# Kernel tuning notes

Measured on AMD Instinct MI355X. Metric: run time of the kernel, lower is better.

The kernel has to match this reference:

```python
import jax, jax.numpy as jnp
import numpy as np
from jax import lax

B, N, D = 32, 256, 128  # graphs, nodes-per-graph, embed_dim
T = B * N               # total nodes


def _mlp(x, W1, b1, W2, b2):
    # Linear -> ReLU -> Linear (query_proj / key_proj)
    return jnp.maximum(x @ W1.T + b1, 0.0) @ W2.T + b2


def _l2norm(x):
    # F.normalize(dim=-1), eps=1e-12
    return x / jnp.maximum(jnp.linalg.norm(x, axis=-1, keepdims=True), 1e-12)


def _gru_cell(x, h, W_ih, W_hh, b_ih, b_hh):
    # torch.nn.GRU single-step cell, gate order (r, z, n)
    gi = x @ W_ih.T + b_ih
    gh = h @ W_hh.T + b_hh
    ir, iz, inn = jnp.split(gi, 3, axis=-1)
    hr, hz, hn = jnp.split(gh, 3, axis=-1)
    r = jax.nn.sigmoid(ir + hr)
    z = jax.nn.sigmoid(iz + hz)
    n = jnp.tanh(inn + r * hn)
    return (1.0 - z) * n + z * h


def setup_inputs() -> dict:
    key = jax.random.key(0)
    ks = jax.random.split(key, 16)
    s = float(1.0 / np.sqrt(D))
    u = lambda k, sh: jax.random.uniform(k, sh, jnp.float32, -s, s)
    return {
        "node_embeddings": jax.random.normal(ks[0], (T, D), jnp.float32),
        "start_nodes": jnp.arange(B, dtype=jnp.int32) * N,  # first node of each graph
        "batch_idx": jnp.repeat(jnp.arange(B, dtype=jnp.int32), N),
        "Wq1": u(ks[1], (D, D)), "bq1": u(ks[2], (D,)),
        "Wq2": u(ks[3], (D, D)), "bq2": u(ks[4], (D,)),
        "Wk1": u(ks[5], (D, D)), "bk1": u(ks[6], (D,)),
        "Wk2": u(ks[7], (D, D)), "bk2": u(ks[8], (D,)),
        "W_ih": u(ks[9], (3 * D, D)), "W_hh": u(ks[10], (3 * D, D)),
        "b_ih": u(ks[11], (3 * D,)), "b_hh": u(ks[12], (3 * D,)),
        "v": jax.random.normal(ks[13], (D,), jnp.float32),
        "Wh": u(ks[14], (D, D)), "bh": u(ks[15], (D,)),
    }


def reference(node_embeddings, start_nodes, batch_idx, Wq1, bq1, Wq2, bq2,
              Wk1, bk1, Wk2, bk2, W_ih, W_hh, b_ih, b_hh, v, Wh, bh):
    Bn = start_nodes.shape[0]
    Tn = node_embeddings.shape[0]
    steps = Tn // Bn - 1  # equal-size graphs: N-1 decode steps after start node

    # graph contexts = per-graph mean of node embeddings -> hidden init
    ones = jnp.ones((Tn,), jnp.float32)
    counts = jax.ops.segment_sum(ones, batch_idx, num_segments=Bn)
    gctx = jax.ops.segment_sum(node_embeddings, batch_idx, num_segments=Bn) / counts[:, None]
    hidden0 = gctx @ Wh.T + bh                       # [B, D]

    # keys are recomputed identically every step in torch; hoist (same math)
    keys = _l2norm(_mlp(node_embeddings, Wk1, bk1, Wk2, bk2))  # [T, D]
    member = batch_idx[None, :] == jnp.arange(Bn)[:, None]     # [B, T]

    def step(carry, _):
        hidden, current, mask = carry
        mask = mask.at[current].set(False)           # visit current nodes
        x = node_embeddings[current]                 # [B, D]
        h = _gru_cell(x, hidden, W_ih, W_hh, b_ih, b_hh)
        q = _l2norm(_mlp(h, Wq1, bq1, Wq2, bq2))     # [B, D]
        # scores over ALL nodes, then masked to own-graph unvisited (as in torch)
        scores = jnp.einsum('btd,d->bt', jnp.tanh(keys[None] + q[:, None, :]), v)
        valid = member & mask[None, :]
        scores = jnp.where(valid, scores, -jnp.inf)
        probs = jax.nn.softmax(scores, axis=1)
        logp = jnp.log(probs + 1e-10)
        nxt = jnp.argmax(probs, axis=1).astype(current.dtype)  # eval-mode greedy
        lp = jnp.take_along_axis(logp, nxt[:, None], axis=1)[:, 0]
        return (h, nxt, mask), (current, lp)

    init = (hidden0, start_nodes, jnp.ones((Tn,), bool))
    (_, cur, _), (tour_steps, lps) = lax.scan(jax.checkpoint(step), init, None, length=steps)
    tours = jnp.concatenate([tour_steps, cur[None]], axis=0).T  # [B, N]
    log_probs = lps.T                                           # [B, N-1]
    return tours, log_probs
```

## Files before the change

### kernel.cpp

```cpp
#include <hip/hip_runtime.h>
#include <hip/hip_bf16.h>
#include <math.h>

#define DD   128
#define NPG  256
#define NGR  32
#define TTOT 8192
#define LOG2E  1.4426950408889634f
#define LOG2E2 2.8853900817779268f
#define KSTRIDE 264
#define SSTR    268
#define H2A(j)  ((j) + (((j)>>5)<<3))
#define PAD16(j) ((j) + (((j)>>4)<<2))

__device__ __forceinline__ float dot4(float4 a, float4 b){
  return a.x*b.x + a.y*b.y + a.z*b.z + a.w*b.w;
}
template<int CTRL, int RMASK>
__device__ __forceinline__ float upd_f(float oldv, float x){
  return __int_as_float(__builtin_amdgcn_update_dpp(
      __float_as_int(oldv), __float_as_int(x), CTRL, RMASK, 0xf, false));
}
__device__ __forceinline__ float dpp_xor1(float x){
  return __int_as_float(__builtin_amdgcn_mov_dpp(__float_as_int(x), 0xB1, 0xf, 0xf, false));
}
__device__ __forceinline__ float dpp_xor2(float x){
  return __int_as_float(__builtin_amdgcn_mov_dpp(__float_as_int(x), 0x4E, 0xf, 0xf, false));
}
__device__ __forceinline__ float quad_sum_dpp(float x){
  float s = x + dpp_xor1(x);
  return s + dpp_xor2(s);
}
__device__ __forceinline__ float dpp_wave_sum(float x){
  x += upd_f<0x111,0xf>(0.f, x);
  x += upd_f<0x112,0xf>(0.f, x);
  x += upd_f<0x114,0xf>(0.f, x);
  x += upd_f<0x118,0xf>(0.f, x);
  x += upd_f<0x142,0xa>(0.f, x);
  x += upd_f<0x143,0xc>(0.f, x);
  return __uint_as_float(__builtin_amdgcn_readlane(__float_as_uint(x), 63));
}
__device__ __forceinline__ float dpp_wave_max(float x){
  const float NI = -INFINITY;
  x = fmaxf(x, upd_f<0x111,0xf>(NI, x));
  x = fmaxf(x, upd_f<0x112,0xf>(NI, x));
  x = fmaxf(x, upd_f<0x114,0xf>(NI, x));
  x = fmaxf(x, upd_f<0x118,0xf>(NI, x));
  x = fmaxf(x, upd_f<0x142,0xa>(NI, x));
  x = fmaxf(x, upd_f<0x143,0xc>(NI, x));
  return __uint_as_float(__builtin_amdgcn_readlane(__float_as_uint(x), 63));
}
__device__ __forceinline__ float sigfast(float x){
  return __builtin_amdgcn_rcpf(1.f + __builtin_amdgcn_exp2f(-x*LOG2E));
}
__device__ __forceinline__ float tanhfast(float y){
  return 1.f - 2.f*__builtin_amdgcn_rcpf(1.f + __builtin_amdgcn_exp2f(y*LOG2E2));
}


__device__ __forceinline__ void load_w128(float* Ws, const float* __restrict__ W, int t){
  const float4* src = (const float4*)W;
  #pragma unroll
  for (int m=0;m<16;m++){
    int idx = m*256+t; int r = idx>>5, c4 = idx&31;
    float4 val = src[idx];
    float* dst = &Ws[r*129 + c4*4];
    dst[0]=val.x; dst[1]=val.y; dst[2]=val.z; dst[3]=val.w;
  }
}

__device__ __forceinline__ void mm_tile(const float* __restrict__ inS, const float* __restrict__ Ws,
                                        float acc[4][4], int jg, int ng){
  #pragma unroll
  for(int r=0;r<4;r++)
    #pragma unroll
    for(int c=0;c<4;c++) acc[r][c]=0.f;
  #pragma unroll 4
  for (int k=0;k<128;k++){
    float w[4], x[4];
    #pragma unroll
    for (int r=0;r<4;r++) w[r] = Ws[(jg*4+r)*129+k];
    #pragma unroll
    for (int c=0;c<4;c++) x[c] = inS[(ng*4+c)*129+k];
    #pragma unroll
    for (int r=0;r<4;r++)
      #pragma unroll
      for (int c=0;c<4;c++) acc[r][c] += w[r]*x[c];
  }
}

__global__ __launch_bounds__(256) void precompute_kernel(
    const float* __restrict__ emb,
    const float* __restrict__ Wk1, const float* __restrict__ bk1,
    const float* __restrict__ Wk2, const float* __restrict__ bk2,
    const float* __restrict__ Wih, const float* __restrict__ bih,
    float* __restrict__ keysE, float* __restrict__ giall)
{
  __shared__ __align__(16) float xs[32*129];
  __shared__ __align__(16) float Ws[128*129];
  __shared__ __align__(16) float hs[32*129];
  __shared__ __align__(16) float os[32*129];
  __shared__ float nrm[32];
  const int t  = threadIdx.x;
  const int n0 = blockIdx.x * 32;
  const int ng = t & 7, jg = t >> 3;

  {
    const float4* src = (const float4*)emb + (size_t)n0*32;
    #pragma unroll
    for (int m=0;m<4;m++){
      int idx = m*256+t; int n = idx>>5, c4 = idx&31;
      float4 val = src[idx];
      float* dst = &xs[n*129 + c4*4];
      dst[0]=val.x; dst[1]=val.y; dst[2]=val.z; dst[3]=val.w;
    }
  }
  load_w128(Ws, Wk1, t);
  __syncthreads();
  {
    float acc[4][4];
    mm_tile(xs, Ws, acc, jg, ng);
    #pragma unroll
    for (int r=0;r<4;r++){
      float bb = bk1[jg*4+r];
      #pragma unroll
      for (int c=0;c<4;c++) hs[(ng*4+c)*129 + jg*4+r] = fmaxf(acc[r][c]+bb, 0.f);
    }
  }
  __syncthreads();
  load_w128(Ws, Wk2, t);
  __syncthreads();
  {
    float acc[4][4];
    mm_tile(hs, Ws, acc, jg, ng);
    #pragma unroll
    for (int r=0;r<4;r++){
      float bb = bk2[jg*4+r];
      #pragma unroll
      for (int c=0;c<4;c++) os[(ng*4+c)*129 + jg*4+r] = acc[r][c]+bb;
    }
  }
  __syncthreads();
  if (t<32){
    float ss=0.f;
    for (int j=0;j<128;j++){ float x = os[t*129+j]; ss += x*x; }
    nrm[t] = fmaxf(sqrtf(ss), 1e-12f);
  }
  __syncthreads();
  #pragma unroll
  for (int m=0;m<16;m++){
    int idx = m*256+t; int nl = idx & 31, d = idx >> 5;
    float kk = os[nl*129 + d] / nrm[nl];
    keysE[(size_t)d*TTOT + n0 + nl] = __builtin_amdgcn_exp2f(kk * LOG2E2);
  }
  for (int c=0;c<3;c++){
    __syncthreads();
    load_w128(Ws, Wih + c*16384, t);
    __syncthreads();
    float acc[4][4];
    mm_tile(xs, Ws, acc, jg, ng);
    #pragma unroll
    for (int r=0;r<4;r++){
      float bb = bih[c*128 + jg*4+r];
      #pragma unroll
      for (int cc=0;cc<4;cc++)
        giall[(size_t)(n0 + ng*4+cc)*384 + c*128 + jg*4 + r] = acc[r][cc] + bb;
    }
  }
}


__global__ __launch_bounds__(512, 2) void decode_kernel(
    const float* __restrict__ emb,
    const float* __restrict__ keysE, const float* __restrict__ giall,
    const float* __restrict__ Whh, const float* __restrict__ bhh,
    const float* __restrict__ Wq1, const float* __restrict__ bq1,
    const float* __restrict__ Wq2, const float* __restrict__ bq2,
    const float* __restrict__ v,   const float* __restrict__ Wh,
    const float* __restrict__ bh,  const int* __restrict__ start_nodes,
    float* __restrict__ tours_o, float* __restrict__ lp_o)
{
  __shared__ __align__(16) float keys_s[128*KSTRIDE];
  __shared__ __align__(16) float h_s[2][160];
  __shared__ __align__(16) float qh_s[160];
  __shared__ __align__(16) float q_s[160];
  __shared__ __align__(16) float v_sp[160];
  __shared__ __align__(16) float spartS[8*SSTR];
  __shared__ int col2node_s[256], node2col_s[256];
  __shared__ float red2[8];

  const int t = threadIdx.x;
  const int b = blockIdx.x;
  const int g  = t >> 2, s3 = t & 3;
  const int w  = t >> 6, L  = t & 63;
  const int oct = L & 7, dgrp = L >> 3;

  float4 whh4[3][8], wq14[8], wq24[8];
  {
    const float4* w0  = (const float4*)(Whh + (size_t)(g      )*128 + s3*32);
    const float4* w1  = (const float4*)(Whh + (size_t)(128 + g)*128 + s3*32);
    const float4* w2  = (const float4*)(Whh + (size_t)(256 + g)*128 + s3*32);
    const float4* q1p = (const float4*)(Wq1 + (size_t)g*128 + s3*32);
    const float4* q2p = (const float4*)(Wq2 + (size_t)g*128 + s3*32);
    #pragma unroll
    for (int i=0;i<8;i++){
      whh4[0][i]=w0[i]; whh4[1][i]=w1[i]; whh4[2][i]=w2[i];
      wq14[i]=q1p[i];   wq24[i]=q2p[i];
    }
  }
  const float br = bhh[g], bz = bhh[128+g], bn = bhh[256+g];
  const float b1g = bq1[g], b2g = bq2[g];

  if (t<128) v_sp[PAD16(t)] = -2.f * v[t];
  if (t<256){ col2node_s[t] = t; node2col_s[t] = t; }
  {
    #pragma unroll
    for (int m=0;m<16;m++){
      int idx = m*512 + t; int d = idx>>6, q = idx&63;
      *(float4*)(keys_s + d*KSTRIDE + q*4) =
        *(const float4*)(keysE + (size_t)d*TTOT + b*256 + q*4);
    }
  }
  {
    int d = t & 127, part = t >> 7;
    float a = 0.f;
    const float* base = emb + (size_t)(b*256 + part*64)*128 + d;
    for (int i=0;i<64;i++) a += base[(size_t)i*128];
    spartS[part*128+d] = a;
  }
  int cur = start_nodes[b];
  __syncthreads();
  if (t<128){
    float a = 0.f;
    #pragma unroll
    for (int p=0;p<4;p++) a += spartS[p*128+t];
    q_s[t] = a * (1.f/256.f);
  }
  __syncthreads();
  if (t<128){
    float a = bh[t];
    const float* wr = Wh + (size_t)t*128;
    for (int k=0;k<128;k++) a += wr[k]*q_s[k];
    h_s[0][H2A(t)] = a;
  }
  {
    float xv = (t<128) ? v[t] : 0.f;
    float tot = dpp_wave_sum(xv);
    if (L==0) red2[w] = tot;
  }
  __syncthreads();
  float sv = 0.f;
  #pragma unroll
  for (int i=0;i<8;i++) sv += red2[i];

  float gir=0.f, giz=0.f, gin=0.f;
  if (s3==0){
    const float* gp = giall + (size_t)cur*384 + g;
    gir = gp[0]; giz = gp[128]; gin = gp[256];
  }

  for (int step=0; step<255; step++){
    const int par = step & 1;
    const int V   = 255 - step;
    const int curl = cur - b*256;

    if (t >= 128 && t < 256){
      int r = t - 128;
      int px = node2col_s[curl];
      keys_s[r*KSTRIDE + px] = keys_s[r*KSTRIDE + V];
    }
    if (t == 384) tours_o[b*256+step] = (float)cur;

    {
      float a0=0.f,a1=0.f,a2=0.f;
      const float4* hc4 = (const float4*)(h_s[par] + s3*40);
      #pragma unroll
      for (int i=0;i<8;i++){
        float4 hv = hc4[i];
        a0 += dot4(whh4[0][i], hv);
        a1 += dot4(whh4[1][i], hv);
        a2 += dot4(whh4[2][i], hv);
      }
      a0 = quad_sum_dpp(a0);
      a1 = quad_sum_dpp(a1);
      a2 = quad_sum_dpp(a2);
      if (s3==0){
        float r = sigfast(gir + a0 + br);
        float z = sigfast(giz + a1 + bz);
        float n = tanhfast(gin + r*(a2 + bn));
        h_s[par^1][H2A(g)] = (1.f-z)*n + z*h_s[par][H2A(g)];
      }
    }
    __syncthreads();

    if (t == 448){
      int px = node2col_s[curl];
      int ln = col2node_s[V];
      col2node_s[px] = ln;
      node2col_s[ln] = px;
    }

    {
      float a=0.f;
      const float4* hc4 = (const float4*)(h_s[par^1] + s3*40);
      #pragma unroll
      for (int i=0;i<8;i++) a += dot4(wq14[i], hc4[i]);
      a = quad_sum_dpp(a);
      if (s3==0) qh_s[H2A(g)] = fmaxf(a + b1g, 0.f);
    }
    __syncthreads();

    {
      float a=0.f;
      const float4* qc4 = (const float4*)(qh_s + s3*40);
      #pragma unroll
      for (int i=0;i<8;i++) a += dot4(wq24[i], qc4[i]);
      a = quad_sum_dpp(a);
      float qval = a + b2g;
      if (s3==0) q_s[PAD16(g)] = qval;
      float ssp = (s3==0) ? qval*qval : 0.f;
      float tot = dpp_wave_sum(ssp);
      if (L==0) red2[w] = tot;
    }
    __syncthreads();

    if (32*w < V){
      float ss = 0.f;
      #pragma unroll
      for (int i=0;i<8;i++) ss += red2[i];
      float rn = 1.f / fmaxf(sqrtf(ss), 1e-12f);
      const float* kbase = keys_s + dgrp*16*KSTRIDE + 32*w + oct*4;
      const float* qb    = q_s  + dgrp*20;
      const float* vbase = v_sp + dgrp*20;
      float4 acc = {0.f,0.f,0.f,0.f};
      #pragma unroll
      for (int jj=0;jj<16;jj++){
        float eqj = __builtin_amdgcn_exp2f(qb[jj] * rn * LOG2E2);
        float vj  = vbase[jj];
        float4 K = *(const float4*)(kbase + jj*KSTRIDE);
        float r0 = __builtin_amdgcn_rcpf(fmaf(K.x, eqj, 1.f));
        float r1 = __builtin_amdgcn_rcpf(fmaf(K.y, eqj, 1.f));
        float r2 = __builtin_amdgcn_rcpf(fmaf(K.z, eqj, 1.f));
        float r3 = __builtin_amdgcn_rcpf(fmaf(K.w, eqj, 1.f));
        acc.x = fmaf(vj, r0, acc.x);
        acc.y = fmaf(vj, r1, acc.y);
        acc.z = fmaf(vj, r2, acc.z);
        acc.w = fmaf(vj, r3, acc.w);
      }
      *(float4*)(spartS + dgrp*SSTR + 32*w + oct*4) = acc;
    }
    __syncthreads();

    {
      const float* sp = spartS + 4*L;
      float sx=0.f, sy=0.f, sz=0.f, sw=0.f;
      #pragma unroll
      for (int i=0;i<8;i++){
        float4 p = *(const float4*)(sp + i*SSTR);
        sx += p.x; sy += p.y; sz += p.z; sw += p.w;
      }
      int c0 = 4*L;
      float vx = (c0+0 < V) ? sv+sx : -INFINITY;
      float vy = (c0+1 < V) ? sv+sy : -INFINITY;
      float vz = (c0+2 < V) ? sv+sz : -INFINITY;
      float vw = (c0+3 < V) ? sv+sw : -INFINITY;
      float bm = vx; int bc = c0;
      if (vy > bm){ bm=vy; bc=c0+1; }
      if (vz > bm){ bm=vz; bc=c0+2; }
      if (vw > bm){ bm=vw; bc=c0+3; }
      float m = dpp_wave_max(bm);
      unsigned long long mk = __ballot(bm == m);
      int flane = __ffsll(mk) - 1;
      int besti = __builtin_amdgcn_readlane(bc, flane);
      float es = __builtin_amdgcn_exp2f((vx-m)*LOG2E) + __builtin_amdgcn_exp2f((vy-m)*LOG2E)
               + __builtin_amdgcn_exp2f((vz-m)*LOG2E) + __builtin_amdgcn_exp2f((vw-m)*LOG2E);
      float S = dpp_wave_sum(es);
      cur = b*256 + col2node_s[besti];
      if (s3==0){
        const float* gp = giall + (size_t)cur*384 + g;
        gir = gp[0]; giz = gp[128]; gin = gp[256];
      }
      if (t==320) lp_o[b*255+step] = logf(1.f/S + 1e-10f);
    }
  }
  if (t==0) tours_o[b*256+255] = (float)cur;

  (void)oct;
}

extern "C" void kernel_launch(void* const* d_in, const int* in_sizes, int n_in,
                              void* d_out, int out_size, void* d_ws, size_t ws_size,
                              hipStream_t stream) {
  const float* emb  = (const float*)d_in[0];
  const int*   startn = (const int*)d_in[1];
  const float* Wq1 = (const float*)d_in[3];  const float* bq1 = (const float*)d_in[4];
  const float* Wq2 = (const float*)d_in[5];  const float* bq2 = (const float*)d_in[6];
  const float* Wk1 = (const float*)d_in[7];  const float* bk1 = (const float*)d_in[8];
  const float* Wk2 = (const float*)d_in[9];  const float* bk2 = (const float*)d_in[10];
  const float* Wih = (const float*)d_in[11]; const float* Whh = (const float*)d_in[12];
  const float* bih = (const float*)d_in[13]; const float* bhh = (const float*)d_in[14];
  const float* v   = (const float*)d_in[15]; const float* Wh  = (const float*)d_in[16];
  const float* bh  = (const float*)d_in[17];

  float* keysE = (float*)d_ws;
  float* giall = keysE + (size_t)TTOT*DD;

  float* outp = (float*)d_out;

  precompute_kernel<<<256, 256, 0, stream>>>(emb, Wk1, bk1, Wk2, bk2, Wih, bih, keysE, giall);
  decode_kernel<<<NGR, 512, 0, stream>>>(emb, keysE, giall, Whh, bhh, Wq1, bq1, Wq2, bq2,
                                         v, Wh, bh, startn, outp, outp + TTOT);
}
```

Before: 886.4 us.

## Split GRU/MLP matvecs into 8-lane groups handling two rows each

The recurrent matvecs change from 4 lanes per output row (32 columns each) to 8 lanes per pair of rows (16 columns each). Each loaded h/q float4 is now reused across two rows, and the reduction uses DPP row shifts for an 8-lane sum. The per-step LDS reads and the partial-sum bookkeeping in the serial decode loop should shrink. It also skips scoring and partial-sum loads for column quads beyond the remaining valid count V, trading some extra branches and selects for less wasted work.

Result: slower. 935.7 us (+5.6%).

```diff
diff --git a/kernel.cpp b/kernel.cpp
--- a/kernel.cpp
+++ b/kernel.cpp
@@ -27,9 +27,15 @@
 __device__ __forceinline__ float dpp_xor2(float x){
   return __int_as_float(__builtin_amdgcn_mov_dpp(__float_as_int(x), 0x4E, 0xf, 0xf, false));
 }
-__device__ __forceinline__ float quad_sum_dpp(float x){
-  float s = x + dpp_xor1(x);
-  return s + dpp_xor2(s);
+__device__ __forceinline__ float red8_lo(float x){
+  x += dpp_xor1(x); x += dpp_xor2(x);
+  x += upd_f<0x104,0xf>(0.f, x);
+  return x;
+}
+__device__ __forceinline__ float red8_hi(float x){
+  x += dpp_xor1(x); x += dpp_xor2(x);
+  x += upd_f<0x114,0xf>(0.f, x);
+  return x;
 }
 __device__ __forceinline__ float dpp_wave_sum(float x){
   x += upd_f<0x111,0xf>(0.f, x);
@@ -191,25 +197,36 @@
 
   const int t = threadIdx.x;
   const int b = blockIdx.x;
-  const int g  = t >> 2, s3 = t & 3;
   const int w  = t >> 6, L  = t & 63;
+  const int G  = t >> 3, u = t & 7;
+  const int sel = (t >> 2) & 1;
+  const int myrow = 2*G + sel;
+  const int act = ((t & 3) == 0);
   const int oct = L & 7, dgrp = L >> 3;
 
-  float4 whh4[3][8], wq14[8], wq24[8];
-  {
-    const float4* w0  = (const float4*)(Whh + (size_t)(g      )*128 + s3*32);
-    const float4* w1  = (const float4*)(Whh + (size_t)(128 + g)*128 + s3*32);
-    const float4* w2  = (const float4*)(Whh + (size_t)(256 + g)*128 + s3*32);
-    const float4* q1p = (const float4*)(Wq1 + (size_t)g*128 + s3*32);
-    const float4* q2p = (const float4*)(Wq2 + (size_t)g*128 + s3*32);
-    #pragma unroll
-    for (int i=0;i<8;i++){
-      whh4[0][i]=w0[i]; whh4[1][i]=w1[i]; whh4[2][i]=w2[i];
-      wq14[i]=q1p[i];   wq24[i]=q2p[i];
-    }
-  }
-  const float br = bhh[g], bz = bhh[128+g], bn = bhh[256+g];
-  const float b1g = bq1[g], b2g = bq2[g];
+  float4 whh6[6][4], wq14[8], wq24[8];
+  {
+    const float4* p0 = (const float4*)(Whh + (size_t)(2*G      )*128 + u*16);
+    const float4* p1 = (const float4*)(Whh + (size_t)(128+2*G  )*128 + u*16);
+    const float4* p2 = (const float4*)(Whh + (size_t)(256+2*G  )*128 + u*16);
+    const float4* p3 = (const float4*)(Whh + (size_t)(2*G+1    )*128 + u*16);
+    const float4* p4 = (const float4*)(Whh + (size_t)(128+2*G+1)*128 + u*16);
+    const float4* p5 = (const float4*)(Whh + (size_t)(256+2*G+1)*128 + u*16);
+    const float4* q1a = (const float4*)(Wq1 + (size_t)(2*G  )*128 + u*16);
+    const float4* q1b = (const float4*)(Wq1 + (size_t)(2*G+1)*128 + u*16);
+    const float4* q2a = (const float4*)(Wq2 + (size_t)(2*G  )*128 + u*16);
+    const float4* q2b = (const float4*)(Wq2 + (size_t)(2*G+1)*128 + u*16);
+    #pragma unroll
+    for (int i=0;i<4;i++){
+      whh6[0][i]=p0[i]; whh6[1][i]=p1[i]; whh6[2][i]=p2[i];
+      whh6[3][i]=p3[i]; whh6[4][i]=p4[i]; whh6[5][i]=p5[i];
+      wq14[i]=q1a[i]; wq14[4+i]=q1b[i];
+      wq24[i]=q2a[i]; wq24[4+i]=q2b[i];
+    }
+  }
+  const float br = bhh[myrow], bz = bhh[128+myrow], bn = bhh[256+myrow];
+  const float b1g = bq1[myrow], b2g = bq2[myrow];
+  const int hoff = u*16 + (u>>1)*8;
 
   if (t<128) v_sp[PAD16(t)] = -2.f * v[t];
   if (t<256){ col2node_s[t] = t; node2col_s[t] = t; }
@@ -254,8 +271,8 @@
   for (int i=0;i<8;i++) sv += red2[i];
 
   float gir=0.f, giz=0.f, gin=0.f;
-  if (s3==0){
-    const float* gp = giall + (size_t)cur*384 + g;
+  if (act){
+    const float* gp = giall + (size_t)cur*384 + myrow;
     gir = gp[0]; giz = gp[128]; gin = gp[256];
   }
 
@@ -272,23 +289,24 @@
     if (t == 384) tours_o[b*256+step] = (float)cur;
 
     {
-      float a0=0.f,a1=0.f,a2=0.f;
-      const float4* hc4 = (const float4*)(h_s[par] + s3*40);
-      #pragma unroll
-      for (int i=0;i<8;i++){
-        float4 hv = hc4[i];
-        a0 += dot4(whh4[0][i], hv);
-        a1 += dot4(whh4[1][i], hv);
-        a2 += dot4(whh4[2][i], hv);
-      }
-      a0 = quad_sum_dpp(a0);
-      a1 = quad_sum_dpp(a1);
-      a2 = quad_sum_dpp(a2);
-      if (s3==0){
-        float r = sigfast(gir + a0 + br);
-        float z = sigfast(giz + a1 + bz);
-        float n = tanhfast(gin + r*(a2 + bn));
-        h_s[par^1][H2A(g)] = (1.f-z)*n + z*h_s[par][H2A(g)];
+      const float4* hc4 = (const float4*)(h_s[par] + hoff);
+      float4 hv0 = hc4[0], hv1 = hc4[1], hv2 = hc4[2], hv3 = hc4[3];
+      float a0 = dot4(whh6[0][0],hv0)+dot4(whh6[0][1],hv1)+dot4(whh6[0][2],hv2)+dot4(whh6[0][3],hv3);
+      float a1 = dot4(whh6[1][0],hv0)+dot4(whh6[1][1],hv1)+dot4(whh6[1][2],hv2)+dot4(whh6[1][3],hv3);
+      float a2 = dot4(whh6[2][0],hv0)+dot4(whh6[2][1],hv1)+dot4(whh6[2][2],hv2)+dot4(whh6[2][3],hv3);
+      float a3 = dot4(whh6[3][0],hv0)+dot4(whh6[3][1],hv1)+dot4(whh6[3][2],hv2)+dot4(whh6[3][3],hv3);
+      float a4 = dot4(whh6[4][0],hv0)+dot4(whh6[4][1],hv1)+dot4(whh6[4][2],hv2)+dot4(whh6[4][3],hv3);
+      float a5 = dot4(whh6[5][0],hv0)+dot4(whh6[5][1],hv1)+dot4(whh6[5][2],hv2)+dot4(whh6[5][3],hv3);
+      a0 = red8_lo(a0); a1 = red8_lo(a1); a2 = red8_lo(a2);
+      a3 = red8_hi(a3); a4 = red8_hi(a4); a5 = red8_hi(a5);
+      if (act){
+        float gr = sel ? a3 : a0;
+        float gz = sel ? a4 : a1;
+        float gn = sel ? a5 : a2;
+        float r = sigfast(gir + gr + br);
+        float z = sigfast(giz + gz + bz);
+        float n = tanhfast(gin + r*(gn + bn));
+        h_s[par^1][H2A(myrow)] = (1.f-z)*n + z*h_s[par][H2A(myrow)];
       }
     }
     __syncthreads();
@@ -301,24 +319,24 @@
     }
 
     {
-      float a=0.f;
-      const float4* hc4 = (const float4*)(h_s[par^1] + s3*40);
-      #pragma unroll
-      for (int i=0;i<8;i++) a += dot4(wq14[i], hc4[i]);
-      a = quad_sum_dpp(a);
-      if (s3==0) qh_s[H2A(g)] = fmaxf(a + b1g, 0.f);
+      const float4* hc4 = (const float4*)(h_s[par^1] + hoff);
+      float4 hv0 = hc4[0], hv1 = hc4[1], hv2 = hc4[2], hv3 = hc4[3];
+      float a0 = dot4(wq14[0],hv0)+dot4(wq14[1],hv1)+dot4(wq14[2],hv2)+dot4(wq14[3],hv3);
+      float a1 = dot4(wq14[4],hv0)+dot4(wq14[5],hv1)+dot4(wq14[6],hv2)+dot4(wq14[7],hv3);
+      a0 = red8_lo(a0); a1 = red8_hi(a1);
+      if (act) qh_s[H2A(myrow)] = fmaxf((sel ? a1 : a0) + b1g, 0.f);
     }
     __syncthreads();
 
     {
-      float a=0.f;
-      const float4* qc4 = (const float4*)(qh_s + s3*40);
-      #pragma unroll
-      for (int i=0;i<8;i++) a += dot4(wq24[i], qc4[i]);
-      a = quad_sum_dpp(a);
-      float qval = a + b2g;
-      if (s3==0) q_s[PAD16(g)] = qval;
-      float ssp = (s3==0) ? qval*qval : 0.f;
+      const float4* qc4 = (const float4*)(qh_s + hoff);
+      float4 qv0 = qc4[0], qv1 = qc4[1], qv2 = qc4[2], qv3 = qc4[3];
+      float a0 = dot4(wq24[0],qv0)+dot4(wq24[1],qv1)+dot4(wq24[2],qv2)+dot4(wq24[3],qv3);
+      float a1 = dot4(wq24[4],qv0)+dot4(wq24[5],qv1)+dot4(wq24[6],qv2)+dot4(wq24[7],qv3);
+      a0 = red8_lo(a0); a1 = red8_hi(a1);
+      float qval = (sel ? a1 : a0) + b2g;
+      if (act) q_s[PAD16(myrow)] = qval;
+      float ssp = act ? qval*qval : 0.f;
       float tot = dpp_wave_sum(ssp);
       if (L==0) red2[w] = tot;
     }
@@ -329,37 +347,41 @@
       #pragma unroll
       for (int i=0;i<8;i++) ss += red2[i];
       float rn = 1.f / fmaxf(sqrtf(ss), 1e-12f);
-      const float* kbase = keys_s + dgrp*16*KSTRIDE + 32*w + oct*4;
-      const float* qb    = q_s  + dgrp*20;
-      const float* vbase = v_sp + dgrp*20;
-      float4 acc = {0.f,0.f,0.f,0.f};
-      #pragma unroll
-      for (int jj=0;jj<16;jj++){
-        float eqj = __builtin_amdgcn_exp2f(qb[jj] * rn * LOG2E2);
-        float vj  = vbase[jj];
-        float4 K = *(const float4*)(kbase + jj*KSTRIDE);
-        float r0 = __builtin_amdgcn_rcpf(fmaf(K.x, eqj, 1.f));
-        float r1 = __builtin_amdgcn_rcpf(fmaf(K.y, eqj, 1.f));
-        float r2 = __builtin_amdgcn_rcpf(fmaf(K.z, eqj, 1.f));
-        float r3 = __builtin_amdgcn_rcpf(fmaf(K.w, eqj, 1.f));
-        acc.x = fmaf(vj, r0, acc.x);
-        acc.y = fmaf(vj, r1, acc.y);
-        acc.z = fmaf(vj, r2, acc.z);
-        acc.w = fmaf(vj, r3, acc.w);
+      if (32*w + oct*4 < V){
+        const float* kbase = keys_s + dgrp*16*KSTRIDE + 32*w + oct*4;
+        const float* qb    = q_s  + dgrp*20;
+        const float* vbase = v_sp + dgrp*20;
+        float4 acc = {0.f,0.f,0.f,0.f};
+        #pragma unroll
+        for (int jj=0;jj<16;jj++){
+          float eqj = __builtin_amdgcn_exp2f(qb[jj] * rn * LOG2E2);
+          float vj  = vbase[jj];
+          float4 K = *(const float4*)(kbase + jj*KSTRIDE);
+          float r0 = __builtin_amdgcn_rcpf(fmaf(K.x, eqj, 1.f));
+          float r1 = __builtin_amdgcn_rcpf(fmaf(K.y, eqj, 1.f));
+          float r2 = __builtin_amdgcn_rcpf(fmaf(K.z, eqj, 1.f));
+          float r3 = __builtin_amdgcn_rcpf(fmaf(K.w, eqj, 1.f));
+          acc.x = fmaf(vj, r0, acc.x);
+          acc.y = fmaf(vj, r1, acc.y);
+          acc.z = fmaf(vj, r2, acc.z);
+          acc.w = fmaf(vj, r3, acc.w);
+        }
+        *(float4*)(spartS + dgrp*SSTR + 32*w + oct*4) = acc;
       }
-      *(float4*)(spartS + dgrp*SSTR + 32*w + oct*4) = acc;
     }
     __syncthreads();
 
     {
-      const float* sp = spartS + 4*L;
       float sx=0.f, sy=0.f, sz=0.f, sw=0.f;
-      #pragma unroll
-      for (int i=0;i<8;i++){
-        float4 p = *(const float4*)(sp + i*SSTR);
-        sx += p.x; sy += p.y; sz += p.z; sw += p.w;
+      int c0 = 4*L;
+      if (c0 < V){
+        const float* sp = spartS + c0;
+        #pragma unroll
+        for (int i=0;i<8;i++){
+          float4 p = *(const float4*)(sp + i*SSTR);
+          sx += p.x; sy += p.y; sz += p.z; sw += p.w;
+        }
       }
-      int c0 = 4*L;
       float vx = (c0+0 < V) ? sv+sx : -INFINITY;
       float vy = (c0+1 < V) ? sv+sy : -INFINITY;
       float vz = (c0+2 < V) ? sv+sz : -INFINITY;
@@ -376,16 +398,14 @@
                + __builtin_amdgcn_exp2f((vz-m)*LOG2E) + __builtin_amdgcn_exp2f((vw-m)*LOG2E);
       float S = dpp_wave_sum(es);
       cur = b*256 + col2node_s[besti];
-      if (s3==0){
-        const float* gp = giall + (size_t)cur*384 + g;
+      if (act){
+        const float* gp = giall + (size_t)cur*384 + myrow;
         gir = gp[0]; giz = gp[128]; gin = gp[256];
       }
       if (t==320) lp_o[b*255+step] = logf(1.f/S + 1e-10f);
     }
   }
   if (t==0) tours_o[b*256+255] = (float)cur;
-
-  (void)oct;
 }
 
 extern "C" void kernel_launch(void* const* d_in, const int* in_sizes, int n_in,
```
